# Kernel tuning notes

Measured on AMD Instinct MI355X. Metric: run time of the kernel, lower is better.

## Reference

```python
import jax, jax.numpy as jnp
import numpy as np

N_RES = 768
C_Z = 128
C_MID = 128
EQUATION = 'ikc,jkc->ijc'
EPS = 1e-5


def layer_norm(x, w, b):
    mu = jnp.mean(x, axis=-1, keepdims=True)
    var = jnp.var(x, axis=-1, keepdims=True)
    return (x - mu) * jax.lax.rsqrt(var + EPS) * w + b


def setup_inputs() -> dict:
    key = jax.random.key(0)
    ks = jax.random.split(key, 16)
    s = 0.02
    inp = {
        'act': jax.random.normal(ks[0], (N_RES, N_RES, C_Z), dtype=jnp.float32),
        'mask': jnp.ones((N_RES, N_RES), dtype=jnp.float32),
        'ln_in_w': jnp.ones((C_Z,), jnp.float32),
        'ln_in_b': jnp.zeros((C_Z,), jnp.float32),
        'W_lp': jax.random.normal(ks[1], (C_Z, C_MID), jnp.float32) * s,
        'b_lp': jnp.zeros((C_MID,), jnp.float32),
        'W_rp': jax.random.normal(ks[2], (C_Z, C_MID), jnp.float32) * s,
        'b_rp': jnp.zeros((C_MID,), jnp.float32),
        'W_lg': jax.random.normal(ks[3], (C_Z, C_MID), jnp.float32) * s,
        'b_lg': jnp.zeros((C_MID,), jnp.float32),
        'W_rg': jax.random.normal(ks[4], (C_Z, C_MID), jnp.float32) * s,
        'b_rg': jnp.zeros((C_MID,), jnp.float32),
        'ln_c_w': jnp.ones((C_MID,), jnp.float32),
        'ln_c_b': jnp.zeros((C_MID,), jnp.float32),
        'W_out': jax.random.normal(ks[5], (C_MID, C_Z), jnp.float32) * s,
        'b_out': jnp.zeros((C_Z,), jnp.float32),
        'W_g': jax.random.normal(ks[6], (C_Z, C_Z), jnp.float32) * s,
        'b_g': jnp.zeros((C_Z,), jnp.float32),
    }
    return inp


def reference(act, mask, ln_in_w, ln_in_b, W_lp, b_lp, W_rp, b_rp,
              W_lg, b_lg, W_rg, b_rg, ln_c_w, ln_c_b, W_out, b_out, W_g, b_g):
    m = mask[..., None]                       # [N, N, 1]
    x = layer_norm(act, ln_in_w, ln_in_b)     # [N, N, c_z]
    input_act = x
    left = m * (x @ W_lp + b_lp) * jax.nn.sigmoid(x @ W_lg + b_lg)
    right = m * (x @ W_rp + b_rp) * jax.nn.sigmoid(x @ W_rg + b_rg)
    # triangular update: [N,N,c] x [N,N,c] -> [N,N,c], contract over k
    out = jnp.einsum(EQUATION, left, right)
    out = layer_norm(out, ln_c_w, ln_c_b)
    out = (out @ W_out + b_out) * jax.nn.sigmoid(input_act @ W_g + b_g)
    return out
```

## Files before the change

kernel.cpp:

```cpp
#include <hip/hip_runtime.h>

#define NR 768
#define CZ 128
#define NNF (768*768)

typedef __bf16 bf16;
typedef __bf16 bf16x8 __attribute__((ext_vector_type(8)));
typedef __bf16 bf16x4 __attribute__((ext_vector_type(4)));
typedef float  f32x4  __attribute__((ext_vector_type(4)));

__device__ __forceinline__ void cp16(void* lds, const void* g) {
    __builtin_amdgcn_global_load_lds(
        (const __attribute__((address_space(1))) void*)g,
        (__attribute__((address_space(3))) void*)lds, 16, 0, 0);
}

__device__ __forceinline__ float sigmoidf_(float x) {
    return 1.f / (1.f + __expf(-x));
}

__global__ __launch_bounds__(256, 2)
void k1_ln_proj(const float* __restrict__ act,  const float* __restrict__ mask,
                const float* __restrict__ lnw,  const float* __restrict__ lnb,
                const float* __restrict__ W0,   const float* __restrict__ W1,
                const float* __restrict__ W2,   const float* __restrict__ W3,
                const float* __restrict__ W4,
                const float* __restrict__ b0,   const float* __restrict__ b1,
                const float* __restrict__ b2,   const float* __restrict__ b3,
                const float* __restrict__ b4,
                bf16* __restrict__ leftT, bf16* __restrict__ rightT,
                bf16* __restrict__ gate)
{
    __shared__ bf16 sXh[64*136];
    __shared__ bf16 sWt[128*136];
    __shared__ bf16 sStage[128*68];
    __shared__ float sSum[64], sSsq[64], sMask[64];

    const int tid = threadIdx.x;
    const int r0  = blockIdx.x * 64;
    const int g32 = tid >> 5;
    const int l32 = tid & 31;
    const int col = l32 * 4;

    float4 v[8];
#pragma unroll
    for (int it = 0; it < 8; ++it) {
        int row = it*8 + g32;
        v[it] = *(const float4*)(act + (size_t)(r0+row)*CZ + col);
        float s = v[it].x + v[it].y + v[it].z + v[it].w;
        float q = v[it].x*v[it].x + v[it].y*v[it].y + v[it].z*v[it].z + v[it].w*v[it].w;
#pragma unroll
        for (int off = 16; off > 0; off >>= 1) {
            s += __shfl_down(s, off, 32);
            q += __shfl_down(q, off, 32);
        }
        if (l32 == 0) { sSum[row] = s; sSsq[row] = q; }
    }
    if (tid < 64) sMask[tid] = mask[r0 + tid];
    __syncthreads();

    {
        float4 w4 = *(const float4*)(lnw + col);
        float4 b4 = *(const float4*)(lnb + col);
#pragma unroll
        for (int it = 0; it < 8; ++it) {
            int row = it*8 + g32;
            float mu  = sSum[row] * (1.f/CZ);
            float var = sSsq[row] * (1.f/CZ) - mu*mu;
            float rs  = rsqrtf(var + 1e-5f);
            bf16x4 o;
            o[0] = (bf16)((v[it].x - mu)*rs*w4.x + b4.x);
            o[1] = (bf16)((v[it].y - mu)*rs*w4.y + b4.y);
            o[2] = (bf16)((v[it].z - mu)*rs*w4.z + b4.z);
            o[3] = (bf16)((v[it].w - mu)*rs*w4.w + b4.w);
            *(bf16x4*)(sXh + row*136 + col) = o;
        }
    }

    const float* Ws[5] = {W0, W1, W2, W3, W4};
    const float* bs[5] = {b0, b1, b2, b3, b4};
    const int wv = tid >> 6, lane = tid & 63, l16 = lane & 15, quad = lane >> 4;

    f32x4 accP[8];
    for (int wi = 0; wi < 5; ++wi) {
        __syncthreads();
        const float* W = Ws[wi];
#pragma unroll
        for (int i = 0; i < 16; ++i) {
            int chunk = tid + i*256;
            int kk = chunk >> 5;
            int nb = (chunk & 31) * 4;
            float4 w = *(const float4*)(W + kk*CZ + nb);
            sWt[(nb+0)*136 + kk] = (bf16)w.x;
            sWt[(nb+1)*136 + kk] = (bf16)w.y;
            sWt[(nb+2)*136 + kk] = (bf16)w.z;
            sWt[(nb+3)*136 + kk] = (bf16)w.w;
        }
        __syncthreads();

        f32x4 acc[8];
        f32x4 zero = {0.f, 0.f, 0.f, 0.f};
#pragma unroll
        for (int t = 0; t < 8; ++t) acc[t] = zero;
#pragma unroll
        for (int ks = 0; ks < 4; ++ks) {
            bf16x8 af = *(const bf16x8*)(sXh + (wv*16 + l16)*136 + ks*32 + quad*8);
#pragma unroll
            for (int t = 0; t < 8; ++t) {
                bf16x8 bfr = *(const bf16x8*)(sWt + (t*16 + l16)*136 + ks*32 + quad*8);
                acc[t] = __builtin_amdgcn_mfma_f32_16x16x32_bf16(af, bfr, acc[t], 0, 0, 0);
            }
        }

        if (wi == 0 || wi == 2) {
#pragma unroll
            for (int t = 0; t < 8; ++t) accP[t] = acc[t];
        } else if (wi == 1 || wi == 3) {
            bf16* dst = (wi == 1) ? leftT : rightT;
#pragma unroll
            for (int t = 0; t < 8; ++t) {
                int c = t*16 + l16;
                float bp = bs[wi-1][c];
                float bg = bs[wi][c];
#pragma unroll
                for (int r = 0; r < 4; ++r) {
                    int m = wv*16 + quad*4 + r;
                    float val = sMask[m] * (accP[t][r] + bp) * sigmoidf_(acc[t][r] + bg);
                    sStage[c*68 + m] = (bf16)val;
                }
            }
            __syncthreads();
#pragma unroll
            for (int i = 0; i < 8; ++i) {
                int chunk = tid + i*256;
                int c = chunk >> 4, u = chunk & 15;
                *(bf16x4*)(dst + (size_t)c*NNF + r0 + u*4) =
                    *(const bf16x4*)(sStage + c*68 + u*4);
            }
        } else {
#pragma unroll
            for (int t = 0; t < 8; ++t) {
                int c = t*16 + l16;
                float bg = bs[4][c];
#pragma unroll
                for (int r = 0; r < 4; ++r) {
                    int m = wv*16 + quad*4 + r;
                    sStage[m*132 + c] = (bf16)sigmoidf_(acc[t][r] + bg);
                }
            }
            __syncthreads();
#pragma unroll
            for (int i = 0; i < 8; ++i) {
                int chunk = tid + i*256;
                int m = chunk >> 5, c4 = chunk & 31;
                *(bf16x4*)(gate + (size_t)(r0+m)*CZ + c4*4) =
                    *(const bf16x4*)(sStage + m*132 + c4*4);
            }
        }
    }
}

__global__ __launch_bounds__(256, 2)
void k2_einsum(const bf16* __restrict__ Lt, const bf16* __restrict__ Rt,
               bf16* __restrict__ Mid)
{
    __shared__ bf16 sA[128*32];
    __shared__ bf16 sB[128*32];

    const int tid = threadIdx.x;
    const int bj = blockIdx.x, bi = blockIdx.y, c = blockIdx.z;
    const size_t cb = (size_t)c * NNF;
    const bf16* Ab = Lt + cb + (size_t)bi * 128 * NR;
    const bf16* Bb = Rt + cb + (size_t)bj * 128 * NR;

    const int wv = tid >> 6, lane = tid & 63, l16 = lane & 15, quad = lane >> 4;
    const int m0 = (wv >> 1) * 64, n0 = (wv & 1) * 64;

    const int q0 = tid, q1 = tid + 256;
    const int ra0 = q0 >> 2, kc0 = (q0 & 3) * 8;
    const int ra1 = q1 >> 2, kc1 = (q1 & 3) * 8;
    bf16* lbA0 = sA + (size_t)(wv*64) * 8;
    bf16* lbA1 = sA + (size_t)(256 + wv*64) * 8;
    bf16* lbB0 = sB + (size_t)(wv*64) * 8;
    bf16* lbB1 = sB + (size_t)(256 + wv*64) * 8;

    f32x4 acc[4][4];
    f32x4 zero = {0.f, 0.f, 0.f, 0.f};
#pragma unroll
    for (int mi = 0; mi < 4; ++mi)
#pragma unroll
        for (int ni = 0; ni < 4; ++ni) acc[mi][ni] = zero;

    for (int ko = 0; ko < NR; ko += 32) {
        __syncthreads();
        cp16(lbA0, Ab + (size_t)ra0*NR + ko + kc0);
        cp16(lbA1, Ab + (size_t)ra1*NR + ko + kc1);
        cp16(lbB0, Bb + (size_t)ra0*NR + ko + kc0);
        cp16(lbB1, Bb + (size_t)ra1*NR + ko + kc1);
        __syncthreads();

        bf16x8 af[4], bfr[4];
#pragma unroll
        for (int i = 0; i < 4; ++i) {
            af[i]  = *(const bf16x8*)(sA + (m0 + i*16 + l16)*32 + quad*8);
            bfr[i] = *(const bf16x8*)(sB + (n0 + i*16 + l16)*32 + quad*8);
        }
#pragma unroll
        for (int mi = 0; mi < 4; ++mi)
#pragma unroll
            for (int ni = 0; ni < 4; ++ni)
                acc[mi][ni] = __builtin_amdgcn_mfma_f32_16x16x32_bf16(
                                  af[mi], bfr[ni], acc[mi][ni], 0, 0, 0);
    }

    bf16* Ob = Mid + cb + (size_t)(bi*128) * NR + bj*128;
#pragma unroll
    for (int mi = 0; mi < 4; ++mi)
#pragma unroll
        for (int ni = 0; ni < 4; ++ni) {
            int colv = n0 + ni*16 + l16;
#pragma unroll
            for (int r = 0; r < 4; ++r) {
                int row = m0 + mi*16 + quad*4 + r;
                Ob[(size_t)row*NR + colv] = (bf16)acc[mi][ni][r];
            }
        }
}

__global__ __launch_bounds__(256, 2)
void k3_ln_out(const bf16* __restrict__ Mid, const bf16* __restrict__ gate,
               const float* __restrict__ lnw, const float* __restrict__ lnb,
               const float* __restrict__ Wout, const float* __restrict__ bout,
               float* __restrict__ out)
{
    __shared__ bf16 sT[128*68];
    __shared__ bf16 sXh[64*136];
    __shared__ bf16 sWt[128*136];
    __shared__ float sMu[64], sRs[64];

    const int tid = threadIdx.x;
    const size_t p0 = (size_t)blockIdx.x * 64;

#pragma unroll
    for (int i = 0; i < 8; ++i) {
        int chunk = tid + i*256;
        int c = chunk >> 4, u = chunk & 15;
        *(bf16x4*)(sT + c*68 + u*4) =
            *(const bf16x4*)(Mid + (size_t)c*NNF + p0 + u*4);
    }
#pragma unroll
    for (int i = 0; i < 16; ++i) {
        int chunk = tid + i*256;
        int kk = chunk >> 5;
        int nb = (chunk & 31) * 4;
        float4 w = *(const float4*)(Wout + kk*CZ + nb);
        sWt[(nb+0)*136 + kk] = (bf16)w.x;
        sWt[(nb+1)*136 + kk] = (bf16)w.y;
        sWt[(nb+2)*136 + kk] = (bf16)w.z;
        sWt[(nb+3)*136 + kk] = (bf16)w.w;
    }
    __syncthreads();

    {
        int pos = tid >> 2, part = tid & 3;
        float s = 0.f, q = 0.f;
#pragma unroll
        for (int j = 0; j < 32; ++j) {
            float x = (float)sT[(part*32 + j)*68 + pos];
            s += x; q += x*x;
        }
        s += __shfl_xor(s, 1); q += __shfl_xor(q, 1);
        s += __shfl_xor(s, 2); q += __shfl_xor(q, 2);
        if (part == 0) {
            float mu  = s * (1.f/CZ);
            float var = q * (1.f/CZ) - mu*mu;
            sMu[pos] = mu;
            sRs[pos] = rsqrtf(var + 1e-5f);
        }
    }
    __syncthreads();

#pragma unroll
    for (int i2 = 0; i2 < 8; ++i2) {
        int id = tid + i2*256;
        int pos = id & 63, c4 = id >> 6;
        float mu = sMu[pos], rs = sRs[pos];
        float4 w = *(const float4*)(lnw + c4*4);
        float4 b = *(const float4*)(lnb + c4*4);
        bf16x4 o;
        o[0] = (bf16)(((float)sT[(c4*4+0)*68 + pos] - mu)*rs*w.x + b.x);
        o[1] = (bf16)(((float)sT[(c4*4+1)*68 + pos] - mu)*rs*w.y + b.y);
        o[2] = (bf16)(((float)sT[(c4*4+2)*68 + pos] - mu)*rs*w.z + b.z);
        o[3] = (bf16)(((float)sT[(c4*4+3)*68 + pos] - mu)*rs*w.w + b.w);
        *(bf16x4*)(sXh + pos*136 + c4*4) = o;
    }
    __syncthreads();

    const int wv = tid >> 6, lane = tid & 63, l16 = lane & 15, quad = lane >> 4;
    f32x4 acc[8];
    f32x4 zero = {0.f, 0.f, 0.f, 0.f};
#pragma unroll
    for (int t = 0; t < 8; ++t) acc[t] = zero;
#pragma unroll
    for (int ks = 0; ks < 4; ++ks) {
        bf16x8 af = *(const bf16x8*)(sXh + (wv*16 + l16)*136 + ks*32 + quad*8);
#pragma unroll
        for (int t = 0; t < 8; ++t) {
            bf16x8 bfr = *(const bf16x8*)(sWt + (t*16 + l16)*136 + ks*32 + quad*8);
            acc[t] = __builtin_amdgcn_mfma_f32_16x16x32_bf16(af, bfr, acc[t], 0, 0, 0);
        }
    }
#pragma unroll
    for (int t = 0; t < 8; ++t) {
        int c = t*16 + l16;
        float bo = bout[c];
#pragma unroll
        for (int r = 0; r < 4; ++r) {
            int m = wv*16 + quad*4 + r;
            size_t p = p0 + m;
            float g = (float)gate[p*CZ + c];
            out[p*CZ + c] = (acc[t][r] + bo) * g;
        }
    }
}

extern "C" void kernel_launch(void* const* d_in, const int* in_sizes, int n_in,
                              void* d_out, int out_size, void* d_ws, size_t ws_size,
                              hipStream_t stream)
{
    const float* act     = (const float*)d_in[0];
    const float* mask    = (const float*)d_in[1];
    const float* ln_in_w = (const float*)d_in[2];
    const float* ln_in_b = (const float*)d_in[3];
    const float* W_lp    = (const float*)d_in[4];
    const float* b_lp    = (const float*)d_in[5];
    const float* W_rp    = (const float*)d_in[6];
    const float* b_rp    = (const float*)d_in[7];
    const float* W_lg    = (const float*)d_in[8];
    const float* b_lg    = (const float*)d_in[9];
    const float* W_rg    = (const float*)d_in[10];
    const float* b_rg    = (const float*)d_in[11];
    const float* ln_c_w  = (const float*)d_in[12];
    const float* ln_c_b  = (const float*)d_in[13];
    const float* W_out   = (const float*)d_in[14];
    const float* b_out   = (const float*)d_in[15];
    const float* W_g     = (const float*)d_in[16];
    const float* b_g     = (const float*)d_in[17];

    char* ws = (char*)d_ws;
    const size_t SZ = (size_t)NNF * CZ * sizeof(bf16);
    bf16* leftT  = (bf16*)(ws);
    bf16* rightT = (bf16*)(ws + SZ);
    bf16* gatev  = (bf16*)(ws + 2*SZ);
    bf16* Mid    = (bf16*)(ws + 3*SZ);
    (void)ws_size; (void)in_sizes; (void)n_in; (void)out_size;

    k1_ln_proj<<<NNF/64, 256, 0, stream>>>(act, mask, ln_in_w, ln_in_b,
        W_lp, W_lg, W_rp, W_rg, W_g,
        b_lp, b_lg, b_rp, b_rg, b_g,
        leftT, rightT, gatev);

    k2_einsum<<<dim3(6, 6, 128), 256, 0, stream>>>(leftT, rightT, Mid);

    k3_ln_out<<<NNF/64, 256, 0, stream>>>(Mid, gatev, ln_c_w, ln_c_b,
        W_out, b_out, (float*)d_out);
}
```

Baseline: 1.875 ms.

## Pretranspose projection weights and split projection kernel by branch with larger tiles

Adds a small kernel that converts and transposes the five projection weight matrices to bf16 once per call, so the projection kernel no longer transposes fp32 weights into LDS inside every block. The projection kernel now handles 128 rows per block and splits into three branches on a grid dimension (left, right, gate). Each branch computes its projection and gate matmuls together over a 64x64 per-wave tile, staging weights with direct global-to-LDS copies. In exchange, every branch block redoes the input load and layernorm, so act is read three times, and register pressure from the 32 accumulators may lower occupancy.

```diff
diff --git a/kernel.cpp b/kernel.cpp
--- a/kernel.cpp
+++ b/kernel.cpp
@@ -19,34 +19,47 @@
     return 1.f / (1.f + __expf(-x));
 }
 
+__global__ void k0_wt(const float* __restrict__ W0, const float* __restrict__ W1,
+                      const float* __restrict__ W2, const float* __restrict__ W3,
+                      const float* __restrict__ W4, bf16* __restrict__ Wt)
+{
+    const float* Ws[5] = {W0, W1, W2, W3, W4};
+    const float* W = Ws[blockIdx.x];
+    bf16* dst = Wt + blockIdx.x * 16384;
+#pragma unroll 4
+    for (int i = 0; i < 64; ++i) {
+        int idx = i*256 + threadIdx.x;
+        int k = idx >> 7, n = idx & 127;
+        dst[n*128 + k] = (bf16)W[idx];
+    }
+}
+
 __global__ __launch_bounds__(256, 2)
-void k1_ln_proj(const float* __restrict__ act,  const float* __restrict__ mask,
-                const float* __restrict__ lnw,  const float* __restrict__ lnb,
-                const float* __restrict__ W0,   const float* __restrict__ W1,
-                const float* __restrict__ W2,   const float* __restrict__ W3,
-                const float* __restrict__ W4,
-                const float* __restrict__ b0,   const float* __restrict__ b1,
-                const float* __restrict__ b2,   const float* __restrict__ b3,
-                const float* __restrict__ b4,
-                bf16* __restrict__ leftT, bf16* __restrict__ rightT,
-                bf16* __restrict__ gate)
+void k1_proj(const float* __restrict__ act,  const float* __restrict__ mask,
+             const float* __restrict__ lnw,  const float* __restrict__ lnb,
+             const bf16*  __restrict__ Wt,
+             const float* __restrict__ b_lp, const float* __restrict__ b_lg,
+             const float* __restrict__ b_rp, const float* __restrict__ b_rg,
+             const float* __restrict__ b_g,
+             bf16* __restrict__ leftT, bf16* __restrict__ rightT,
+             bf16* __restrict__ gate)
 {
-    __shared__ bf16 sXh[64*136];
-    __shared__ bf16 sWt[128*136];
-    __shared__ bf16 sStage[128*68];
-    __shared__ float sSum[64], sSsq[64], sMask[64];
-
-    const int tid = threadIdx.x;
-    const int r0  = blockIdx.x * 64;
-    const int g32 = tid >> 5;
-    const int l32 = tid & 31;
+    __shared__ bf16 sXh[128*136];
+    __shared__ bf16 sB0[128*32];
+    __shared__ bf16 sB1[128*32];
+    __shared__ float sMask[128], sSum[128], sSsq[128];
+
+    const int tid    = threadIdx.x;
+    const int branch = blockIdx.x;
+    const size_t p0  = (size_t)blockIdx.y * 128;
+
+    const int l32 = tid & 31, g8 = tid >> 5;
     const int col = l32 * 4;
-
-    float4 v[8];
-#pragma unroll
-    for (int it = 0; it < 8; ++it) {
-        int row = it*8 + g32;
-        v[it] = *(const float4*)(act + (size_t)(r0+row)*CZ + col);
+    float4 v[16];
+#pragma unroll
+    for (int it = 0; it < 16; ++it) {
+        int row = it*8 + g8;
+        v[it] = *(const float4*)(act + (p0+row)*CZ + col);
         float s = v[it].x + v[it].y + v[it].z + v[it].w;
         float q = v[it].x*v[it].x + v[it].y*v[it].y + v[it].z*v[it].z + v[it].w*v[it].w;
 #pragma unroll
@@ -56,15 +69,14 @@
         }
         if (l32 == 0) { sSum[row] = s; sSsq[row] = q; }
     }
-    if (tid < 64) sMask[tid] = mask[r0 + tid];
+    if (tid < 128) sMask[tid] = mask[p0 + tid];
     __syncthreads();
-
     {
         float4 w4 = *(const float4*)(lnw + col);
         float4 b4 = *(const float4*)(lnb + col);
 #pragma unroll
-        for (int it = 0; it < 8; ++it) {
-            int row = it*8 + g32;
+        for (int it = 0; it < 16; ++it) {
+            int row = it*8 + g8;
             float mu  = sSum[row] * (1.f/CZ);
             float var = sSsq[row] * (1.f/CZ) - mu*mu;
             float rs  = rsqrtf(var + 1e-5f);
@@ -77,85 +89,110 @@
         }
     }
 
-    const float* Ws[5] = {W0, W1, W2, W3, W4};
-    const float* bs[5] = {b0, b1, b2, b3, b4};
+    const bf16 *Bp, *Bg = nullptr;
+    const float *bpb, *bgb = nullptr;
+    if (branch == 0)      { Bp = Wt;          Bg = Wt + 16384;   bpb = b_lp; bgb = b_lg; }
+    else if (branch == 1) { Bp = Wt + 32768;  Bg = Wt + 49152;   bpb = b_rp; bgb = b_rg; }
+    else                  { Bp = Wt + 65536;                     bpb = b_g; }
+
     const int wv = tid >> 6, lane = tid & 63, l16 = lane & 15, quad = lane >> 4;
-
-    f32x4 accP[8];
-    for (int wi = 0; wi < 5; ++wi) {
-        __syncthreads();
-        const float* W = Ws[wi];
+    const int m0 = (wv >> 1) * 64, n0 = (wv & 1) * 64;
+
+    const int q0 = tid, q1 = tid + 256;
+    const int nr0 = q0 >> 2, kc0 = (q0 & 3) * 8;
+    const int nr1 = q1 >> 2, kc1 = (q1 & 3) * 8;
+    bf16* lb0a = sB0 + (wv*64)*8;
+    bf16* lb0b = sB0 + (256 + wv*64)*8;
+    bf16* lb1a = sB1 + (wv*64)*8;
+    bf16* lb1b = sB1 + (256 + wv*64)*8;
+
+    f32x4 accP[4][4], accG[4][4];
+    f32x4 zero = {0.f, 0.f, 0.f, 0.f};
+#pragma unroll
+    for (int mi = 0; mi < 4; ++mi)
+#pragma unroll
+        for (int ni = 0; ni < 4; ++ni) { accP[mi][ni] = zero; accG[mi][ni] = zero; }
+
+    for (int ks = 0; ks < 4; ++ks) {
+        __syncthreads();
+        cp16(lb0a, Bp + nr0*128 + ks*32 + kc0);
+        cp16(lb0b, Bp + nr1*128 + ks*32 + kc1);
+        if (branch < 2) {
+            cp16(lb1a, Bg + nr0*128 + ks*32 + kc0);
+            cp16(lb1b, Bg + nr1*128 + ks*32 + kc1);
+        }
+        __syncthreads();
+
+        bf16x8 af[4], bp_[4], bg_[4];
+#pragma unroll
+        for (int i = 0; i < 4; ++i) {
+            af[i]  = *(const bf16x8*)(sXh + (m0 + i*16 + l16)*136 + ks*32 + quad*8);
+            bp_[i] = *(const bf16x8*)(sB0 + (n0 + i*16 + l16)*32 + quad*8);
+        }
+        if (branch < 2) {
+#pragma unroll
+            for (int i = 0; i < 4; ++i)
+                bg_[i] = *(const bf16x8*)(sB1 + (n0 + i*16 + l16)*32 + quad*8);
+        }
+#pragma unroll
+        for (int mi = 0; mi < 4; ++mi)
+#pragma unroll
+            for (int ni = 0; ni < 4; ++ni) {
+                accP[mi][ni] = __builtin_amdgcn_mfma_f32_16x16x32_bf16(
+                                   af[mi], bp_[ni], accP[mi][ni], 0, 0, 0);
+                if (branch < 2)
+                    accG[mi][ni] = __builtin_amdgcn_mfma_f32_16x16x32_bf16(
+                                       af[mi], bg_[ni], accG[mi][ni], 0, 0, 0);
+            }
+    }
+
+    __syncthreads();
+    bf16* sT = sXh;
+    if (branch < 2) {
+        bf16* dst = (branch == 0) ? leftT : rightT;
+#pragma unroll
+        for (int ni = 0; ni < 4; ++ni) {
+            int c = n0 + ni*16 + l16;
+            float bp = bpb[c];
+            float bg = bgb[c];
+#pragma unroll
+            for (int mi = 0; mi < 4; ++mi)
+#pragma unroll
+                for (int r = 0; r < 4; ++r) {
+                    int m = m0 + mi*16 + quad*4 + r;
+                    float val = sMask[m] * (accP[mi][ni][r] + bp)
+                                         * sigmoidf_(accG[mi][ni][r] + bg);
+                    sT[c*132 + m] = (bf16)val;
+                }
+        }
+        __syncthreads();
 #pragma unroll
         for (int i = 0; i < 16; ++i) {
             int chunk = tid + i*256;
-            int kk = chunk >> 5;
-            int nb = (chunk & 31) * 4;
-            float4 w = *(const float4*)(W + kk*CZ + nb);
-            sWt[(nb+0)*136 + kk] = (bf16)w.x;
-            sWt[(nb+1)*136 + kk] = (bf16)w.y;
-            sWt[(nb+2)*136 + kk] = (bf16)w.z;
-            sWt[(nb+3)*136 + kk] = (bf16)w.w;
-        }
-        __syncthreads();
-
-        f32x4 acc[8];
-        f32x4 zero = {0.f, 0.f, 0.f, 0.f};
-#pragma unroll
-        for (int t = 0; t < 8; ++t) acc[t] = zero;
-#pragma unroll
-        for (int ks = 0; ks < 4; ++ks) {
-            bf16x8 af = *(const bf16x8*)(sXh + (wv*16 + l16)*136 + ks*32 + quad*8);
-#pragma unroll
-            for (int t = 0; t < 8; ++t) {
-                bf16x8 bfr = *(const bf16x8*)(sWt + (t*16 + l16)*136 + ks*32 + quad*8);
-                acc[t] = __builtin_amdgcn_mfma_f32_16x16x32_bf16(af, bfr, acc[t], 0, 0, 0);
-            }
-        }
-
-        if (wi == 0 || wi == 2) {
-#pragma unroll
-            for (int t = 0; t < 8; ++t) accP[t] = acc[t];
-        } else if (wi == 1 || wi == 3) {
-            bf16* dst = (wi == 1) ? leftT : rightT;
-#pragma unroll
-            for (int t = 0; t < 8; ++t) {
-                int c = t*16 + l16;
-                float bp = bs[wi-1][c];
-                float bg = bs[wi][c];
+            int c = chunk >> 5, u = chunk & 31;
+            *(bf16x4*)(dst + (size_t)c*NNF + p0 + u*4) =
+                *(const bf16x4*)(sT + c*132 + u*4);
+        }
+    } else {
+#pragma unroll
+        for (int ni = 0; ni < 4; ++ni) {
+            int c = n0 + ni*16 + l16;
+            float bg = bpb[c];
+#pragma unroll
+            for (int mi = 0; mi < 4; ++mi)
 #pragma unroll
                 for (int r = 0; r < 4; ++r) {
-                    int m = wv*16 + quad*4 + r;
-                    float val = sMask[m] * (accP[t][r] + bp) * sigmoidf_(acc[t][r] + bg);
-                    sStage[c*68 + m] = (bf16)val;
+                    int m = m0 + mi*16 + quad*4 + r;
+                    sT[m*132 + c] = (bf16)sigmoidf_(accP[mi][ni][r] + bg);
                 }
-            }
-            __syncthreads();
-#pragma unroll
-            for (int i = 0; i < 8; ++i) {
-                int chunk = tid + i*256;
-                int c = chunk >> 4, u = chunk & 15;
-                *(bf16x4*)(dst + (size_t)c*NNF + r0 + u*4) =
-                    *(const bf16x4*)(sStage + c*68 + u*4);
-            }
-        } else {
-#pragma unroll
-            for (int t = 0; t < 8; ++t) {
-                int c = t*16 + l16;
-                float bg = bs[4][c];
-#pragma unroll
-                for (int r = 0; r < 4; ++r) {
-                    int m = wv*16 + quad*4 + r;
-                    sStage[m*132 + c] = (bf16)sigmoidf_(acc[t][r] + bg);
-                }
-            }
-            __syncthreads();
-#pragma unroll
-            for (int i = 0; i < 8; ++i) {
-                int chunk = tid + i*256;
-                int m = chunk >> 5, c4 = chunk & 31;
-                *(bf16x4*)(gate + (size_t)(r0+m)*CZ + c4*4) =
-                    *(const bf16x4*)(sStage + m*132 + c4*4);
-            }
+        }
+        __syncthreads();
+#pragma unroll
+        for (int i = 0; i < 16; ++i) {
+            int chunk = tid + i*256;
+            int m = chunk >> 5, c4 = chunk & 31;
+            *(bf16x4*)(gate + (p0 + m)*CZ + c4*4) =
+                *(const bf16x4*)(sT + m*132 + c4*4);
         }
     }
 }
@@ -353,12 +390,13 @@
     bf16* rightT = (bf16*)(ws + SZ);
     bf16* gatev  = (bf16*)(ws + 2*SZ);
     bf16* Mid    = (bf16*)(ws + 3*SZ);
+    bf16* Wt     = (bf16*)(ws + 3*SZ);
     (void)ws_size; (void)in_sizes; (void)n_in; (void)out_size;
 
-    k1_ln_proj<<<NNF/64, 256, 0, stream>>>(act, mask, ln_in_w, ln_in_b,
-        W_lp, W_lg, W_rp, W_rg, W_g,
-        b_lp, b_lg, b_rp, b_rg, b_g,
-        leftT, rightT, gatev);
+    k0_wt<<<5, 256, 0, stream>>>(W_lp, W_lg, W_rp, W_rg, W_g, Wt);
+
+    k1_proj<<<dim3(3, NNF/128), 256, 0, stream>>>(act, mask, ln_in_w, ln_in_b,
+        Wt, b_lp, b_lg, b_rp, b_rg, b_g, leftT, rightT, gatev);
 
     k2_einsum<<<dim3(6, 6, 128), 256, 0, stream>>>(leftT, rightT, Mid);
 
```

Measured after the change: 1.531 ms. 18.3% less time.
